# Performance work log

Hardware: AMD Instinct MI355X
Metric: run time of the kernel (lower is better)

The kernel has to match this reference:

```python
import jax, jax.numpy as jnp
import numpy as np
import math

IM_SIZE = (256, 256)
OVERSAMP = 1.25
WIDTH = 6
BETA = math.pi * math.sqrt(((WIDTH / OVERSAMP) * (OVERSAMP - 0.5)) ** 2 - 0.8)
OS_SIZE = tuple(int(math.ceil(OVERSAMP * n)) for n in IM_SIZE)
N_COILS = 8
N_PTS = 1 << 20


def _i0(x):
    # Abramowitz & Stegun polynomial approximation of I0 (matches sigpy's
    # kaiser_bessel kernel); differentiable, safe branches via where-trick.
    xs = jnp.where(x < 3.75, x, 0.0)
    y = (xs / 3.75) ** 2
    small = 1.0 + y * (3.5156229 + y * (3.0899424 + y * (1.2067492
            + y * (0.2659732 + y * (0.0360768 + y * 0.0045813)))))
    xl = jnp.where(x < 3.75, 3.75, x)
    t = 3.75 / xl
    large = (jnp.exp(xl) / jnp.sqrt(xl)) * (0.39894228 + t * (0.01328592
            + t * (0.00225319 + t * (-0.00157565 + t * (0.00916281
            + t * (-0.02057706 + t * (0.02635537 + t * (-0.01647633
            + t * 0.00392377))))))))
    return jnp.where(x < 3.75, small, large)


def _kb(x):
    # Kaiser-Bessel interpolation kernel, x in [-1, 1]
    return _i0(BETA * jnp.sqrt(jnp.clip(1.0 - x * x, 0.0, 1.0)))


def _apod_1d(n, os_n):
    idx = jnp.arange(n, dtype=jnp.float32) - n // 2
    a = jnp.sqrt(BETA ** 2 - (np.pi * WIDTH * idx / os_n) ** 2)
    return a / jnp.sinh(a)


def _nufft_forward(img, trj):
    """img: (N, B, ny, nx) complex; trj: (N, K, 2) in [-n/2, n/2]. -> (N, B, K)"""
    ny, nx = IM_SIZE
    oy, ox = OS_SIZE
    # Apodization (de-apodization for KB gridding) + nufft scaling
    apod = _apod_1d(ny, oy)[:, None] * _apod_1d(nx, ox)[None, :]
    x = img * (apod / math.sqrt(ny * nx))
    # Centered zero-pad to oversampled grid
    py, px = oy // 2 - ny // 2, ox // 2 - nx // 2
    x = jnp.pad(x, ((0, 0), (0, 0), (py, oy - ny - py), (px, ox - nx - px)))
    # Centered FFT (ifftshift -> fft -> fftshift), norm=None as in sigpy
    x = jnp.fft.fftshift(
        jnp.fft.fftn(jnp.fft.ifftshift(x, axes=(-2, -1)), axes=(-2, -1)),
        axes=(-2, -1))
    # Scale trajectory to oversampled grid coordinates
    cy = trj[..., 0] * (oy / ny) + oy // 2  # (N, K)
    cx = trj[..., 1] * (ox / nx) + ox // 2
    hw = WIDTH / 2.0
    y0 = jnp.ceil(cy - hw).astype(jnp.int32)
    x0 = jnp.ceil(cx - hw).astype(jnp.int32)

    def interp_one(grid, cy_n, cx_n, y0_n, x0_n):
        # grid: (B, oy, ox); cy_n/cx_n: (K,) -> (B, K)
        acc = jnp.zeros((grid.shape[0],) + cy_n.shape, dtype=grid.dtype)
        for j in range(WIDTH):  # fixed 6x6 KB taps
            yj = y0_n + j
            wy = _kb((yj.astype(jnp.float32) - cy_n) / hw)
            gy = yj % oy
            for l in range(WIDTH):
                xl = x0_n + l
                wx = _kb((xl.astype(jnp.float32) - cx_n) / hw)
                gx = xl % ox
                acc = acc + (wy * wx)[None, :] * grid[:, gy, gx]
        return acc

    ksp = jax.vmap(interp_one)(x, cy, cx, y0, x0)  # (N, B, K)
    return ksp / (WIDTH ** 2)


def setup_inputs() -> dict:
    key = jax.random.key(0)
    k1, k2, k3 = jax.random.split(key, 3)
    img_real = jax.random.normal(k1, (1, N_COILS) + IM_SIZE, dtype=jnp.float32)
    img_imag = jax.random.normal(k2, (1, N_COILS) + IM_SIZE, dtype=jnp.float32)
    scale = jnp.array([IM_SIZE[0], IM_SIZE[1]], dtype=jnp.float32)
    trj = (jax.random.uniform(k3, (1, N_PTS, 2), dtype=jnp.float32) - 0.5) * scale
    return {"img_real": img_real, "img_imag": img_imag, "trj": trj}


def reference(img_real, img_imag, trj):
    ksp = _nufft_forward(img_real + 1j * img_imag, trj)
    # return complex k-space as stacked (real, imag): (N, B, K, 2)
    return jnp.stack([ksp.real, ksp.imag], axis=-1)
```

## Files before the change

kernel.cpp:

```cpp
#include <hip/hip_runtime.h>
#include <math.h>

#define OS    320
#define IMN   256
#define NCOIL 8
#define HS    326
#define HROWB (HS * 32)
#define PI_F  3.14159265358979f
#define BETA_F 10.955108f
#define GSCALE 65536.0f

typedef _Float16 half4  __attribute__((ext_vector_type(4)));
typedef unsigned uint2v __attribute__((ext_vector_type(2)));

__device__ __forceinline__ void fmamix_lo(float& acc, float w, unsigned h) {
    asm("v_fma_mix_f32 %0, %1, %2, %0 op_sel_hi:[0,1,0]"
        : "+v"(acc) : "v"(w), "v"(h));
}
__device__ __forceinline__ void fmamix_hi(float& acc, float w, unsigned h) {
    asm("v_fma_mix_f32 %0, %1, %2, %0 op_sel:[0,1,0] op_sel_hi:[0,1,0]"
        : "+v"(acc) : "v"(w), "v"(h));
}

__device__ __forceinline__ float i0f(float x) {
    if (x < 3.75f) {
        float y = x * (1.0f / 3.75f); y *= y;
        return 1.0f + y*(3.5156229f + y*(3.0899424f + y*(1.2067492f
             + y*(0.2659732f + y*(0.0360768f + y*0.0045813f)))));
    } else {
        float t = 3.75f / x;
        float p = 0.39894228f + t*(0.01328592f + t*(0.00225319f + t*(-0.00157565f
              + t*(0.00916281f + t*(-0.02057706f + t*(0.02635537f + t*(-0.01647633f
              + t*0.00392377f)))))));
        return expf(x) * rsqrtf(x) * p;
    }
}

__device__ __forceinline__ float apod1(int i) {
    float idx = (float)(i - 128);
    float c = PI_F * 6.0f * idx * (1.0f / (float)OS);
    float a = sqrtf(BETA_F * BETA_F - c * c);
    float sh = 0.5f * (expf(a) - expf(-a));
    return a / sh;
}

__global__ void build_lut(float* __restrict__ lut) {
    int i = blockIdx.x * 256 + threadIdx.x;
    if (i <= 1024)
        lut[i] = i0f(BETA_F * sqrtf(1.0f - (float)i * (1.0f / 1024.0f)));
}


#define FFT_STAGES(lds, tw64, cc, bb, jj)                                   \
  {                                                                         \
    int base_ = ((cc) * 5 + (bb)) * 65;                                     \
    _Pragma("unroll")                                                       \
    for (int s_ = 0; s_ < 6; ++s_) {                                        \
      int h_ = 32 >> s_;                                                    \
      int i_ = (jj) & (h_ - 1);                                             \
      int p_ = (((jj) >> (5 - s_)) << (6 - s_)) + i_;                       \
      float2 u_ = lds[base_ + p_];                                          \
      float2 v_ = lds[base_ + p_ + h_];                                     \
      float2 w_ = tw64[i_ << s_];                                           \
      lds[base_ + p_] = make_float2(u_.x + v_.x, u_.y + v_.y);              \
      float dx_ = u_.x - v_.x, dy_ = u_.y - v_.y;                           \
      lds[base_ + p_ + h_] =                                                \
          make_float2(dx_ * w_.x - dy_ * w_.y, dx_ * w_.y + dy_ * w_.x);    \
      __syncthreads();                                                      \
    }                                                                       \
  }

__global__ __launch_bounds__(320) void fft_pass1(const float* __restrict__ imr,
                                                 const float* __restrict__ imi,
                                                 float2* __restrict__ out) {
    __shared__ float2 xg[10 * 65];
    __shared__ float2 tw64[33];
    int iy = blockIdx.x;
    int c0 = blockIdx.y * 2;
    int t  = threadIdx.x;

    if (t < 33) {
        float ang = (float)t * (-2.0f * PI_F / 64.0f);
        tw64[t] = make_float2(cosf(ang), sinf(ang));
    }
    for (int s = t; s < 640; s += 320) {
        int c = s >> 8 >> 6;
        c = (s >= 320) ? 1 : 0;
        int n = s - c * 320;
        int b = n % 5, a = n / 5;
        float2 v = make_float2(0.f, 0.f);
        if (n >= 192 || n < 128) {
            int ix = (n >= 192) ? (n - 192) : (n + 128);
            float ap = apod1(ix);
            int gi = (c0 + c) * (IMN * IMN) + iy * IMN + ix;
            v = make_float2(imr[gi] * ap, imi[gi] * ap);
        }
        xg[(c * 5 + b) * 65 + a] = v;
    }
    __syncthreads();

    {
        int c = t / 160, r = t - c * 160;
        int b = r >> 5, j = r & 31;
        FFT_STAGES(xg, tw64, c, b, j)
    }

    int k = t;
    int rm = __brev((unsigned)(k & 63)) >> 26;
    float ang1 = (float)k * (-2.0f * PI_F / 320.0f);
    float w1r = cosf(ang1), w1i = sinf(ang1);
    float w2r = w1r * w1r - w1i * w1i, w2i = 2.0f * w1r * w1i;
    float w3r = w2r * w1r - w2i * w1i, w3i = w2r * w1i + w2i * w1r;
    float w4r = w2r * w2r - w2i * w2i, w4i = 2.0f * w2r * w2i;
    float ay = apod1(iy) * (1.0f / 256.0f);
    int y = iy + 192; if (y >= OS) y -= OS;
    float Fr[2], Fi[2];
    #pragma unroll
    for (int c = 0; c < 2; ++c) {
        int base = c * 5 * 65;
        float2 g0 = xg[base + rm];
        float2 g1 = xg[base + 65 + rm];
        float2 g2 = xg[base + 130 + rm];
        float2 g3 = xg[base + 195 + rm];
        float2 g4 = xg[base + 260 + rm];
        float fr = g0.x, fi = g0.y;
        fr += g1.x * w1r - g1.y * w1i;  fi += g1.x * w1i + g1.y * w1r;
        fr += g2.x * w2r - g2.y * w2i;  fi += g2.x * w2i + g2.y * w2r;
        fr += g3.x * w3r - g3.y * w3i;  fi += g3.x * w3i + g3.y * w3r;
        fr += g4.x * w4r - g4.y * w4i;  fi += g4.x * w4i + g4.y * w4r;
        Fr[c] = fr * ay; Fi[c] = fi * ay;
    }
    *(float4*)(out + ((size_t)k * OS + y) * NCOIL + c0) =
        make_float4(Fr[0], Fi[0], Fr[1], Fi[1]);
}

__global__ __launch_bounds__(320) void fft_pass2(const float2* __restrict__ in,
                                                 char* __restrict__ gbytes) {
    __shared__ float2 xg[10 * 65];
    __shared__ float2 tw64[33];
    int kx = blockIdx.x;
    int c0 = blockIdx.y * 2;
    int t  = threadIdx.x;

    if (t < 33) {
        float ang = (float)t * (-2.0f * PI_F / 64.0f);
        tw64[t] = make_float2(cosf(ang), sinf(ang));
    }
    const float2* row = in + (size_t)kx * OS * NCOIL + c0;
    for (int s = t; s < 640; s += 320) {
        int c = (s >= 320) ? 1 : 0;
        int n = s - c * 320;
        int b = n % 5, a = n / 5;
        float2 v = make_float2(0.f, 0.f);
        if (n >= 192 || n < 128)
            v = row[n * NCOIL + c];
        xg[(c * 5 + b) * 65 + a] = v;
    }
    __syncthreads();

    {
        int c = t / 160, r = t - c * 160;
        int b = r >> 5, j = r & 31;
        FFT_STAGES(xg, tw64, c, b, j)
    }

    int k = t;
    int rm = __brev((unsigned)(k & 63)) >> 26;
    float ang1 = (float)k * (-2.0f * PI_F / 320.0f);
    float w1r = cosf(ang1), w1i = sinf(ang1);
    float w2r = w1r * w1r - w1i * w1i, w2i = 2.0f * w1r * w1i;
    float w3r = w2r * w1r - w2i * w1i, w3i = w2r * w1i + w2i * w1r;
    float w4r = w2r * w2r - w2i * w2i, w4i = 2.0f * w2r * w2i;
    float Fr[2], Fi[2];
    #pragma unroll
    for (int c = 0; c < 2; ++c) {
        int base = c * 5 * 65;
        float2 g0 = xg[base + rm];
        float2 g1 = xg[base + 65 + rm];
        float2 g2 = xg[base + 130 + rm];
        float2 g3 = xg[base + 195 + rm];
        float2 g4 = xg[base + 260 + rm];
        float fr = g0.x, fi = g0.y;
        fr += g1.x * w1r - g1.y * w1i;  fi += g1.x * w1i + g1.y * w1r;
        fr += g2.x * w2r - g2.y * w2i;  fi += g2.x * w2i + g2.y * w2r;
        fr += g3.x * w3r - g3.y * w3i;  fi += g3.x * w3i + g3.y * w3r;
        fr += g4.x * w4r - g4.y * w4i;  fi += g4.x * w4i + g4.y * w4r;
        Fr[c] = fr * GSCALE; Fi[c] = fi * GSCALE;
    }
    int r = k + 160;  if (r >= OS) r -= OS;
    int c2 = kx + 160; if (c2 >= OS) c2 -= OS;
    half4 hh;
    hh[0] = (_Float16)Fr[0]; hh[1] = (_Float16)Fi[0];
    hh[2] = (_Float16)Fr[1]; hh[3] = (_Float16)Fi[1];
    int hys[2]; int nhy = 1; hys[0] = r + 3;
    if (r < 3)        hys[nhy++] = r + 323;
    else if (r >= 317) hys[nhy++] = r - 317;
    int hxs[2]; int nhx = 1; hxs[0] = c2 + 3;
    if (c2 < 3)        hxs[nhx++] = c2 + 323;
    else if (c2 >= 317) hxs[nhx++] = c2 - 317;
    for (int a = 0; a < nhy; ++a)
        for (int b = 0; b < nhx; ++b)
            *(half4*)(gbytes + (size_t)hys[a] * HROWB + hxs[b] * 32 + c0 * 4) = hh;
}

__global__ __launch_bounds__(256) void interp_kernel(const float* __restrict__ trj,
                                                     const char* __restrict__ gbytes,
                                                     const float* __restrict__ lut,
                                                     float2* __restrict__ out, int K) {
    int tid = blockIdx.x * 256 + threadIdx.x;
    int k = tid >> 3;
    int c = tid & 7;
    int cp = c & 3;
    int tp = c >> 2;
    if (k >= K) return;
    float2 tj = ((const float2*)trj)[k];
    float cy = tj.x * 1.25f + 160.0f;
    float cx = tj.y * 1.25f + 160.0f;
    int y0 = (int)ceilf(cy - 3.0f);
    int x0 = (int)ceilf(cx - 3.0f);
    const char* base0 = gbytes + (size_t)(y0 + 3) * HROWB
                      + (x0 + 3) * 32 + cp * 8 + tp * 32;
    half4 h[18];
    #pragma unroll
    for (int j = 0; j < 6; ++j) {
        const char* rb = base0 + j * HROWB;
        #pragma unroll
        for (int p = 0; p < 3; ++p)
            h[j * 3 + p] = *(const half4*)(rb + p * 64);
    }
    float argu = (c < 6) ? ((float)(y0 + c) - cy) * (1.0f / 3.0f)
                         : ((float)(x0 + (c - 6)) - cx) * (1.0f / 3.0f);
    float argv = ((float)(x0 + 2 + cp) - cx) * (1.0f / 3.0f);
    float tu = fminf(argu * argu * 1024.0f, 1023.0f);
    int   iu = (int)tu;  float fu = tu - (float)iu;
    float a0 = lut[iu], a1 = lut[iu + 1];
    float u = fmaf(fu, a1 - a0, a0);
    float tv = fminf(argv * argv * 1024.0f, 1023.0f);
    int   iv = (int)tv;  float fv = tv - (float)iv;
    float b0 = lut[iv], b1 = lut[iv + 1];
    float v = fmaf(fv, b1 - b0, b0);
    int gb = (threadIdx.x & 63) & 56;
    float wy[6], wx[6];
    wy[0] = __shfl(u, gb + 0); wy[1] = __shfl(u, gb + 1);
    wy[2] = __shfl(u, gb + 2); wy[3] = __shfl(u, gb + 3);
    wy[4] = __shfl(u, gb + 4); wy[5] = __shfl(u, gb + 5);
    wx[0] = __shfl(u, gb + 6); wx[1] = __shfl(u, gb + 7);
    wx[2] = __shfl(v, gb + 0); wx[3] = __shfl(v, gb + 1);
    wx[4] = __shfl(v, gb + 2); wx[5] = __shfl(v, gb + 3);
    float accr0 = 0.f, acci0 = 0.f, accr1 = 0.f, acci1 = 0.f;
    #pragma unroll
    for (int j = 0; j < 6; ++j) {
        float wyj = wy[j];
        #pragma unroll
        for (int p = 0; p < 3; ++p) {
            float w = wyj * wx[2 * p + tp];
            uint2v hu = __builtin_bit_cast(uint2v, h[j * 3 + p]);
            fmamix_lo(accr0, w, hu.x);
            fmamix_hi(acci0, w, hu.x);
            fmamix_lo(accr1, w, hu.y);
            fmamix_hi(acci1, w, hu.y);
        }
    }
    accr0 += __shfl_xor(accr0, 4);
    acci0 += __shfl_xor(acci0, 4);
    accr1 += __shfl_xor(accr1, 4);
    acci1 += __shfl_xor(acci1, 4);
    const float s = 1.0f / (36.0f * GSCALE);
    float2 res = tp ? make_float2(accr1 * s, acci1 * s)
                    : make_float2(accr0 * s, acci0 * s);
    union { float2 f; double d; } ru; ru.f = res;
    __builtin_nontemporal_store(ru.d,
        (double*)(out + (size_t)(2 * cp + tp) * K + k));
}

extern "C" void kernel_launch(void* const* d_in, const int* in_sizes, int n_in,
                              void* d_out, int out_size, void* d_ws, size_t ws_size,
                              hipStream_t stream) {
    const float* imr = (const float*)d_in[0];
    const float* imi = (const float*)d_in[1];
    const float* trj = (const float*)d_in[2];
    int K = in_sizes[2] / 2;

    char* ws = (char*)d_ws;
    float2* buf1  = (float2*)ws;
    char*   gridh = ws + 6553600;
    float*  lut   = (float*)(ws + 9954432);

    (void)n_in; (void)out_size; (void)ws_size;

    build_lut<<<5, 256, 0, stream>>>(lut);
    fft_pass1<<<dim3(IMN, 4), 320, 0, stream>>>(imr, imi, buf1);
    fft_pass2<<<dim3(OS, 4), 320, 0, stream>>>(buf1, gridh);
    interp_kernel<<<(K * NCOIL + 255) / 256, 256, 0, stream>>>(trj, gridh, lut,
                                                               (float2*)d_out, K);
}
```

Measured before the change: 132.0 us.

## Assign four threads per k-space point, each covering two coils over all taps

The interpolation kernel moves from 8 threads per sample (coil pair × half of the x-taps) to 4 threads per sample, each handling two coils across the full 6x6 stencil. This drops the cross-lane shfl_xor reduction and halves the number of threads and trajectory loads, and each thread now issues 36 half4 loads instead of 18. Kernel weights are computed with three LUT lookups per thread and spread via shuffles, and a sched_barrier forces all grid loads to issue before the weight math. The costs are higher register pressure from 36 half4 values, which may lower occupancy, and two strided nontemporal stores per thread instead of one.

```diff
diff --git a/kernel.cpp b/kernel.cpp
--- a/kernel.cpp
+++ b/kernel.cpp
@@ -49,7 +49,6 @@
     if (i <= 1024)
         lut[i] = i0f(BETA_F * sqrtf(1.0f - (float)i * (1.0f / 1024.0f)));
 }
-
 
 #define FFT_STAGES(lds, tw64, cc, bb, jj)                                   \
   {                                                                         \
@@ -84,8 +83,7 @@
         tw64[t] = make_float2(cosf(ang), sinf(ang));
     }
     for (int s = t; s < 640; s += 320) {
-        int c = s >> 8 >> 6;
-        c = (s >= 320) ? 1 : 0;
+        int c = (s >= 320) ? 1 : 0;
         int n = s - c * 320;
         int b = n % 5, a = n / 5;
         float2 v = make_float2(0.f, 0.f);
@@ -208,69 +206,69 @@
                                                      const float* __restrict__ lut,
                                                      float2* __restrict__ out, int K) {
     int tid = blockIdx.x * 256 + threadIdx.x;
-    int k = tid >> 3;
-    int c = tid & 7;
-    int cp = c & 3;
-    int tp = c >> 2;
+    int k  = tid >> 2;
+    int cp = tid & 3;
     if (k >= K) return;
     float2 tj = ((const float2*)trj)[k];
     float cy = tj.x * 1.25f + 160.0f;
     float cx = tj.y * 1.25f + 160.0f;
     int y0 = (int)ceilf(cy - 3.0f);
     int x0 = (int)ceilf(cx - 3.0f);
-    const char* base0 = gbytes + (size_t)(y0 + 3) * HROWB
-                      + (x0 + 3) * 32 + cp * 8 + tp * 32;
-    half4 h[18];
+    const char* base0 = gbytes + (size_t)(y0 + 3) * HROWB + (x0 + 3) * 32 + cp * 8;
+
+    half4 h[36];
     #pragma unroll
     for (int j = 0; j < 6; ++j) {
         const char* rb = base0 + j * HROWB;
         #pragma unroll
-        for (int p = 0; p < 3; ++p)
-            h[j * 3 + p] = *(const half4*)(rb + p * 64);
-    }
-    float argu = (c < 6) ? ((float)(y0 + c) - cy) * (1.0f / 3.0f)
-                         : ((float)(x0 + (c - 6)) - cx) * (1.0f / 3.0f);
-    float argv = ((float)(x0 + 2 + cp) - cx) * (1.0f / 3.0f);
-    float tu = fminf(argu * argu * 1024.0f, 1023.0f);
-    int   iu = (int)tu;  float fu = tu - (float)iu;
-    float a0 = lut[iu], a1 = lut[iu + 1];
-    float u = fmaf(fu, a1 - a0, a0);
-    float tv = fminf(argv * argv * 1024.0f, 1023.0f);
-    int   iv = (int)tv;  float fv = tv - (float)iv;
-    float b0 = lut[iv], b1 = lut[iv + 1];
-    float v = fmaf(fv, b1 - b0, b0);
-    int gb = (threadIdx.x & 63) & 56;
+        for (int l = 0; l < 6; ++l)
+            h[j * 6 + l] = *(const half4*)(rb + l * 32);
+    }
+    __builtin_amdgcn_sched_barrier(0);
+
+    float argA = ((float)(y0 + cp) - cy) * (1.0f / 3.0f);
+    float argB = ((float)(x0 + cp) - cx) * (1.0f / 3.0f);
+    float argC = (cp < 2) ? ((float)(y0 + 4 + cp) - cy) * (1.0f / 3.0f)
+                          : ((float)(x0 + 2 + cp) - cx) * (1.0f / 3.0f);
+    float tA = fminf(argA * argA * 1024.0f, 1023.0f);
+    int   iA = (int)tA;  float fA = tA - (float)iA;
+    float uA = fmaf(fA, lut[iA + 1] - lut[iA], lut[iA]);
+    float tB = fminf(argB * argB * 1024.0f, 1023.0f);
+    int   iB = (int)tB;  float fB = tB - (float)iB;
+    float uB = fmaf(fB, lut[iB + 1] - lut[iB], lut[iB]);
+    float tC = fminf(argC * argC * 1024.0f, 1023.0f);
+    int   iC = (int)tC;  float fC = tC - (float)iC;
+    float uC = fmaf(fC, lut[iC + 1] - lut[iC], lut[iC]);
+
+    int gb = (threadIdx.x & 63) & 60;
     float wy[6], wx[6];
-    wy[0] = __shfl(u, gb + 0); wy[1] = __shfl(u, gb + 1);
-    wy[2] = __shfl(u, gb + 2); wy[3] = __shfl(u, gb + 3);
-    wy[4] = __shfl(u, gb + 4); wy[5] = __shfl(u, gb + 5);
-    wx[0] = __shfl(u, gb + 6); wx[1] = __shfl(u, gb + 7);
-    wx[2] = __shfl(v, gb + 0); wx[3] = __shfl(v, gb + 1);
-    wx[4] = __shfl(v, gb + 2); wx[5] = __shfl(v, gb + 3);
-    float accr0 = 0.f, acci0 = 0.f, accr1 = 0.f, acci1 = 0.f;
+    wy[0] = __shfl(uA, gb + 0); wy[1] = __shfl(uA, gb + 1);
+    wy[2] = __shfl(uA, gb + 2); wy[3] = __shfl(uA, gb + 3);
+    wx[0] = __shfl(uB, gb + 0); wx[1] = __shfl(uB, gb + 1);
+    wx[2] = __shfl(uB, gb + 2); wx[3] = __shfl(uB, gb + 3);
+    wy[4] = __shfl(uC, gb + 0); wy[5] = __shfl(uC, gb + 1);
+    wx[4] = __shfl(uC, gb + 2); wx[5] = __shfl(uC, gb + 3);
+
+    float r0 = 0.f, i0 = 0.f, r1 = 0.f, i1 = 0.f;
     #pragma unroll
     for (int j = 0; j < 6; ++j) {
         float wyj = wy[j];
         #pragma unroll
-        for (int p = 0; p < 3; ++p) {
-            float w = wyj * wx[2 * p + tp];
-            uint2v hu = __builtin_bit_cast(uint2v, h[j * 3 + p]);
-            fmamix_lo(accr0, w, hu.x);
-            fmamix_hi(acci0, w, hu.x);
-            fmamix_lo(accr1, w, hu.y);
-            fmamix_hi(acci1, w, hu.y);
+        for (int l = 0; l < 6; ++l) {
+            float w = wyj * wx[l];
+            uint2v hu = __builtin_bit_cast(uint2v, h[j * 6 + l]);
+            fmamix_lo(r0, w, hu.x);
+            fmamix_hi(i0, w, hu.x);
+            fmamix_lo(r1, w, hu.y);
+            fmamix_hi(i1, w, hu.y);
         }
     }
-    accr0 += __shfl_xor(accr0, 4);
-    acci0 += __shfl_xor(acci0, 4);
-    accr1 += __shfl_xor(accr1, 4);
-    acci1 += __shfl_xor(acci1, 4);
     const float s = 1.0f / (36.0f * GSCALE);
-    float2 res = tp ? make_float2(accr1 * s, acci1 * s)
-                    : make_float2(accr0 * s, acci0 * s);
-    union { float2 f; double d; } ru; ru.f = res;
-    __builtin_nontemporal_store(ru.d,
-        (double*)(out + (size_t)(2 * cp + tp) * K + k));
+    union { float2 f; double d; } u0, u1;
+    u0.f = make_float2(r0 * s, i0 * s);
+    u1.f = make_float2(r1 * s, i1 * s);
+    __builtin_nontemporal_store(u0.d, (double*)(out + (size_t)(2 * cp) * K + k));
+    __builtin_nontemporal_store(u1.d, (double*)(out + (size_t)(2 * cp + 1) * K + k));
 }
 
 extern "C" void kernel_launch(void* const* d_in, const int* in_sizes, int n_in,
@@ -291,6 +289,6 @@
     build_lut<<<5, 256, 0, stream>>>(lut);
     fft_pass1<<<dim3(IMN, 4), 320, 0, stream>>>(imr, imi, buf1);
     fft_pass2<<<dim3(OS, 4), 320, 0, stream>>>(buf1, gridh);
-    interp_kernel<<<(K * NCOIL + 255) / 256, 256, 0, stream>>>(trj, gridh, lut,
-                                                               (float2*)d_out, K);
-}
+    interp_kernel<<<(K * 4 + 255) / 256, 256, 0, stream>>>(trj, gridh, lut,
+                                                           (float2*)d_out, K);
+}
```

New measurement: 126.4 us. 4.3% less time.
